# Performance work log

Hardware: AMD Instinct MI355X
Metric: run time of the kernel (lower is better)

The kernel has to match this reference:

```python
import jax, jax.numpy as jnp
from jax import lax
import numpy as np

NEG_INF = -1000000000.0  # matches torch masked_fill value
POS_THRESH = -100000000.0


def setup_inputs() -> dict:
    key = jax.random.key(0)
    k1, k2, k3 = jax.random.split(key, 3)
    B, C_in, L = 1, 16, 2048
    C_out, groups, K = 16, 4, 3
    scores = jax.random.normal(k1, (B, C_in, L, L), dtype=jnp.float32)
    weight = jax.random.normal(k2, (C_out, C_in // groups, K, K), dtype=jnp.float32) * 0.1
    bias = jax.random.normal(k3, (C_out,), dtype=jnp.float32) * 0.1
    return {"scores": scores, "weight": weight, "bias": bias}


def reference(scores, weight, bias):
    B, C_in, L, _ = scores.shape
    C_out, cpg, K, _ = weight.shape
    groups = C_in // cpg
    mask = jnp.tril(jnp.ones((L, L), dtype=bool))[None, None]  # (1,1,L,L) causal

    s = scores.astype(jnp.float32)
    z = jnp.where(mask, s, NEG_INF)

    # sparsemax over last axis: sort desc, cumsum, support-size threshold
    z_sorted = -jnp.sort(-z, axis=-1)                 # descending
    cum_sum = jnp.cumsum(z_sorted, axis=-1)
    k_idx = jnp.arange(1, L + 1, dtype=z.dtype)        # (L,) broadcasts over (B,C,L,L)
    cond = (1.0 + k_idx * z_sorted > cum_sum) & (z_sorted > POS_THRESH)
    k_sp = jnp.sum(cond, axis=-1, keepdims=True)       # support size, int
    k_safe = jnp.maximum(k_sp, 1)
    cum_sum_k = jnp.take_along_axis(cum_sum, k_safe - 1, axis=-1)
    tau = (cum_sum_k - 1.0) / k_safe.astype(z.dtype)
    tau = jnp.where(k_sp == 0, jnp.inf, tau)
    probs = jnp.maximum(z - tau, 0.0)                  # (B,C_in,L,L)

    # grouped same-padded conv2d over the (L,L) score map
    out = lax.conv_general_dilated(
        probs, weight,
        window_strides=(1, 1),
        padding=[(K // 2, K // 2), (K // 2, K // 2)],
        feature_group_count=groups,
        dimension_numbers=("NCHW", "OIHW", "NCHW"),
    )
    out = out + bias[None, :, None, None]
    out = jnp.where(mask, out, 0.0)
    return out.astype(scores.dtype)
```

## Files before the change

kernel.cpp:

```cpp
#include <hip/hip_runtime.h>

#define L 2048
#define CIN 16
#define GROUPS 4
#define NEG_INF  -1000000000.0f
#define POS_THRESH -100000000.0f

__global__ __launch_bounds__(256) void tau_kernel(const float* __restrict__ scores,
                                                  float* __restrict__ tau_out) {
    const int wid  = (blockIdx.x << 2) + (threadIdx.x >> 6);
    const int lane = threadIdx.x & 63;
    const int ws   = threadIdx.x >> 6;
    const int ch   = wid >> 11;
    const int row  = wid & 2047;
    const int n    = row + 1;
    const float* zrow = scores + ((size_t)ch * L + row) * L;

    float v[32];
    float m = NEG_INF;
#pragma unroll
    for (int j = 0; j < 8; ++j) {
        int c4 = lane + (j << 6);
        int c  = c4 << 2;
        float4 z = make_float4(NEG_INF, NEG_INF, NEG_INF, NEG_INF);
        if (c < n) z = *((const float4*)zrow + c4);
        v[4*j+0] = (c + 0 < n) ? z.x : NEG_INF;
        v[4*j+1] = (c + 1 < n) ? z.y : NEG_INF;
        v[4*j+2] = (c + 2 < n) ? z.z : NEG_INF;
        v[4*j+3] = (c + 3 < n) ? z.w : NEG_INF;
        m = fmaxf(m, fmaxf(fmaxf(v[4*j+0], v[4*j+1]), fmaxf(v[4*j+2], v[4*j+3])));
    }
#pragma unroll
    for (int d = 32; d; d >>= 1) m = fmaxf(m, __shfl_xor(m, d, 64));

    const float thr = m - 1.0f;

    __shared__ float buf[4][64];
    int base = 0;
#pragma unroll
    for (int j = 0; j < 32; ++j) {
        bool p = v[j] > thr;
        unsigned long long mask = __ballot(p);
        if (mask) {
            if (p) {
                int pos = __builtin_amdgcn_mbcnt_lo((unsigned)mask, 0);
                pos = __builtin_amdgcn_mbcnt_hi((unsigned)(mask >> 32), pos);
                pos += base;
                if (pos < 64) buf[ws][pos] = v[j];
            }
            base += __popcll(mask);
        }
    }
    __syncthreads();
    const int cnt = base;

    float tau;
    if (cnt <= 64) {
        float x = (lane < cnt) ? buf[ws][lane] : NEG_INF;
#pragma unroll
        for (int k = 2; k <= 64; k <<= 1) {
#pragma unroll
            for (int j = k >> 1; j > 0; j >>= 1) {
                float p = __shfl_xor(x, j, 64);
                bool desc    = ((lane & k) == 0);
                bool earlier = ((lane & j) == 0);
                float mx = fmaxf(x, p), mn = fminf(x, p);
                x = (desc == earlier) ? mx : mn;
            }
        }
        float csum = x;
#pragma unroll
        for (int d = 1; d < 64; d <<= 1) {
            float y = __shfl_up(csum, d, 64);
            if (lane >= d) csum += y;
        }
        bool cond = (1.0f + (float)(lane + 1) * x > csum) && (x > POS_THRESH);
        unsigned long long cmask = __ballot(cond);
        int k = (int)__popcll(cmask);
        float ck = __shfl(csum, k - 1, 64);
        tau = (ck - 1.0f) / (float)k;
    } else {
        tau = thr;
        int k_prev = -1;
        for (int it = 0; it < 64; ++it) {
            float S = 0.0f, Kf = 0.0f;
#pragma unroll
            for (int j = 0; j < 32; ++j)
                if (v[j] > tau) { S += v[j]; Kf += 1.0f; }
#pragma unroll
            for (int d = 32; d; d >>= 1) {
                S  += __shfl_xor(S,  d, 64);
                Kf += __shfl_xor(Kf, d, 64);
            }
            int K = (int)Kf;
            if (K == k_prev) break;
            tau = (S - 1.0f) / Kf;
            k_prev = K;
        }
    }
    if (lane == 0) tau_out[ch * L + row] = tau;
}

#define TR 16
#define TC 128
#define HR 18
#define PST 132

struct W6 { float l, m0, m1, m2, m3, r; };

__global__ __launch_bounds__(256, 4) void conv_kernel(const float* __restrict__ scores,
                                                      const float* __restrict__ tau,
                                                      const float* __restrict__ weight,
                                                      const float* __restrict__ bias,
                                                      float* __restrict__ out) {
    const int c0 = blockIdx.x * TC;
    const int r0 = blockIdx.y * TR;
    const int g  = blockIdx.z;
    const int t  = threadIdx.x;

    if (c0 > r0 + TR - 1) {
        const float4 z4 = make_float4(0.f, 0.f, 0.f, 0.f);
#pragma unroll
        for (int jj = 0; jj < 8; ++jj) {
            int idx = t + (jj << 8);
            int c4  = idx & 31;
            int r   = (idx >> 5) & 15;
            int o   = idx >> 9;
            float4* p = (float4*)(out + (((size_t)((g << 2) + o) * L + (r0 + r)) * L + c0)) + c4;
            *p = z4;
        }
        return;
    }

    __shared__ __align__(16) float P[4][HR][PST];

    const bool interior = (c0 >= 1) && (c0 + TC + 1 <= r0) && (r0 + TR <= L - 1);

    if (interior) {
        for (int ic = 0; ic < 4; ++ic) {
            const float* sb = scores + (size_t)((g << 2) + ic) * L * L;
            const float* tb = tau + ((g << 2) + ic) * L;
#pragma unroll
            for (int kk = 0; kk < 3; ++kk) {
                int idx = t + (kk << 8);
                if (idx < HR * 32) {
                    int hr = idx >> 5;
                    int c4 = idx & 31;
                    int r  = r0 - 1 + hr;
                    float tv = tb[r];
                    float4 z = *((const float4*)(sb + (size_t)r * L + c0) + c4);
                    float4 val;
                    val.x = fmaxf(z.x - tv, 0.f);
                    val.y = fmaxf(z.y - tv, 0.f);
                    val.z = fmaxf(z.z - tv, 0.f);
                    val.w = fmaxf(z.w - tv, 0.f);
                    *((float4*)&P[ic][hr][c4 << 2]) = val;
                }
            }
        }
        if (t < 144) {
            int side = t & 1, j = t >> 1;
            int ic = j / HR, hr = j - ic * HR;
            int r = r0 - 1 + hr;
            int c = side ? (c0 + TC) : (c0 - 1);
            float tv = tau[((g << 2) + ic) * L + r];
            float z  = scores[((size_t)((g << 2) + ic) * L + r) * L + c];
            P[ic][hr][side ? TC : 131] = fmaxf(z - tv, 0.f);
        }
    } else {
        for (int ic = 0; ic < 4; ++ic) {
            const float* sb = scores + (size_t)((g << 2) + ic) * L * L;
            const float* tb = tau + ((g << 2) + ic) * L;
#pragma unroll
            for (int kk = 0; kk < 3; ++kk) {
                int idx = t + (kk << 8);
                if (idx < HR * 32) {
                    int hr = idx >> 5;
                    int c4 = idx & 31;
                    int r  = r0 - 1 + hr;
                    int cb = c0 + (c4 << 2);
                    float4 val = make_float4(0.f, 0.f, 0.f, 0.f);
                    if (r >= 0 && r < L && cb <= r) {
                        float tv = tb[r];
                        float4 z = *((const float4*)(sb + (size_t)r * L) + (cb >> 2));
                        val.x = fmaxf(z.x - tv, 0.f);
                        val.y = (cb + 1 <= r) ? fmaxf(z.y - tv, 0.f) : 0.f;
                        val.z = (cb + 2 <= r) ? fmaxf(z.z - tv, 0.f) : 0.f;
                        val.w = (cb + 3 <= r) ? fmaxf(z.w - tv, 0.f) : 0.f;
                    }
                    *((float4*)&P[ic][hr][c4 << 2]) = val;
                }
            }
        }
        if (t < 144) {
            int side = t & 1, j = t >> 1;
            int ic = j / HR, hr = j - ic * HR;
            int r = r0 - 1 + hr;
            int c = side ? (c0 + TC) : (c0 - 1);
            float val = 0.f;
            if (r >= 0 && r < L && c >= 0 && c <= r) {
                val = fmaxf(scores[((size_t)((g << 2) + ic) * L + r) * L + c]
                            - tau[((g << 2) + ic) * L + r], 0.f);
            }
            P[ic][hr][side ? TC : 131] = val;
        }
    }
    __syncthreads();

    const int o    = __builtin_amdgcn_readfirstlane(t >> 6);
    const int lane = t & 63;
    const int col4 = lane & 31;
    const int rh   = lane >> 5;
    const int hb   = rh << 3;
    const int go   = (g << 2) + o;
    const int cb   = c0 + (col4 << 2);
    const int li   = col4 ? ((col4 << 2) - 2) : 130;
    const int ri   = (col4 << 2) + 4;

    float w[4][9];
#pragma unroll
    for (int ic = 0; ic < 4; ++ic)
#pragma unroll
        for (int k = 0; k < 9; ++k) w[ic][k] = weight[((go << 2) + ic) * 9 + k];
    const float bb = bias[go];

    auto ldwin = [&](int ic, int hr) -> W6 {
        const float* rp = &P[ic][hr][0];
        float4 M  = *(const float4*)(rp + (col4 << 2));
        float2 Lv = *(const float2*)(rp + li);
        float2 Rv = *(const float2*)(rp + ri);
        W6 q; q.l = Lv.y; q.m0 = M.x; q.m1 = M.y; q.m2 = M.z; q.m3 = M.w; q.r = Rv.x;
        return q;
    };

    float4 acc[8];
#pragma unroll
    for (int rr = 0; rr < 8; ++rr) acc[rr] = make_float4(bb, bb, bb, bb);

#pragma unroll
    for (int ic = 0; ic < 4; ++ic) {
        W6 a = ldwin(ic, hb);
        W6 b = ldwin(ic, hb + 1);
#pragma unroll
        for (int rr = 0; rr < 8; ++rr) {
            W6 c = ldwin(ic, hb + rr + 2);
            const W6 rows[3] = { a, b, c };
#pragma unroll
            for (int dy = 0; dy < 3; ++dy) {
                const W6& q = rows[dy];
                const float w0 = w[ic][dy * 3 + 0];
                const float w1 = w[ic][dy * 3 + 1];
                const float w2 = w[ic][dy * 3 + 2];
                acc[rr].x = fmaf(q.l,  w0, fmaf(q.m0, w1, fmaf(q.m1, w2, acc[rr].x)));
                acc[rr].y = fmaf(q.m0, w0, fmaf(q.m1, w1, fmaf(q.m2, w2, acc[rr].y)));
                acc[rr].z = fmaf(q.m1, w0, fmaf(q.m2, w1, fmaf(q.m3, w2, acc[rr].z)));
                acc[rr].w = fmaf(q.m2, w0, fmaf(q.m3, w1, fmaf(q.r,  w2, acc[rr].w)));
            }
            a = b; b = c;
        }
    }

    float* outp = out + ((size_t)go * L + (r0 + hb)) * L + cb;
    if (interior) {
#pragma unroll
        for (int rr = 0; rr < 8; ++rr)
            *(float4*)(outp + (size_t)rr * L) = acc[rr];
    } else {
#pragma unroll
        for (int rr = 0; rr < 8; ++rr) {
            int r = r0 + hb + rr;
            float4 res;
            res.x = (cb     <= r) ? acc[rr].x : 0.f;
            res.y = (cb + 1 <= r) ? acc[rr].y : 0.f;
            res.z = (cb + 2 <= r) ? acc[rr].z : 0.f;
            res.w = (cb + 3 <= r) ? acc[rr].w : 0.f;
            *(float4*)(outp + (size_t)rr * L) = res;
        }
    }
}

extern "C" void kernel_launch(void* const* d_in, const int* in_sizes, int n_in,
                              void* d_out, int out_size, void* d_ws, size_t ws_size,
                              hipStream_t stream) {
    const float* scores = (const float*)d_in[0];
    const float* weight = (const float*)d_in[1];
    const float* bias   = (const float*)d_in[2];
    float* out = (float*)d_out;
    float* tau = (float*)d_ws;

    tau_kernel<<<(CIN * L) / 4, 256, 0, stream>>>(scores, tau);

    dim3 gridB(L / TC, L / TR, GROUPS);
    conv_kernel<<<gridB, 256, 0, stream>>>(scores, tau, weight, bias, out);
}
```

Baseline: 526.0 us.

## Halve conv tile width and batch all halo loads before LDS writes

The conv tile shrinks from 128 to 64 columns, each thread now computes 4 rows instead of 8, and the launch-bound occupancy target rises from 4 to 8 blocks. Staging is restructured so every global load for all four input channels is issued into registers first, then converted and written to shared memory, which gives more memory-level parallelism per block. The aim is better latency hiding through higher occupancy and more loads in flight. The cost is a larger relative halo overhead per tile and more blocks to schedule.

Measured after the change: 496.3 us. -5.7%, faster.

```diff
diff --git a/kernel.cpp b/kernel.cpp
--- a/kernel.cpp
+++ b/kernel.cpp
@@ -102,13 +102,13 @@
 }
 
 #define TR 16
-#define TC 128
+#define TC 64
 #define HR 18
-#define PST 132
+#define PST 68
 
 struct W6 { float l, m0, m1, m2, m3, r; };
 
-__global__ __launch_bounds__(256, 4) void conv_kernel(const float* __restrict__ scores,
+__global__ __launch_bounds__(256, 8) void conv_kernel(const float* __restrict__ scores,
                                                       const float* __restrict__ tau,
                                                       const float* __restrict__ weight,
                                                       const float* __restrict__ bias,
@@ -121,11 +121,11 @@
     if (c0 > r0 + TR - 1) {
         const float4 z4 = make_float4(0.f, 0.f, 0.f, 0.f);
 #pragma unroll
-        for (int jj = 0; jj < 8; ++jj) {
-            int idx = t + (jj << 8);
-            int c4  = idx & 31;
-            int r   = (idx >> 5) & 15;
-            int o   = idx >> 9;
+        for (int jj = 0; jj < 4; ++jj) {
+            int idx = t + (jj << 8);
+            int c4  = idx & 15;
+            int r   = (idx >> 4) & 15;
+            int o   = idx >> 8;
             float4* p = (float4*)(out + (((size_t)((g << 2) + o) * L + (r0 + r)) * L + c0)) + c4;
             *p = z4;
         }
@@ -136,85 +136,107 @@
 
     const bool interior = (c0 >= 1) && (c0 + TC + 1 <= r0) && (r0 + TR <= L - 1);
 
+    const float* sbase = scores + (size_t)(g << 2) * L * L;
+    const float* tbase = tau + (g << 2) * L;
+
+    float4 zr[5];
+    float  tvr[5];
+
     if (interior) {
-        for (int ic = 0; ic < 4; ++ic) {
-            const float* sb = scores + (size_t)((g << 2) + ic) * L * L;
-            const float* tb = tau + ((g << 2) + ic) * L;
-#pragma unroll
-            for (int kk = 0; kk < 3; ++kk) {
-                int idx = t + (kk << 8);
-                if (idx < HR * 32) {
-                    int hr = idx >> 5;
-                    int c4 = idx & 31;
-                    int r  = r0 - 1 + hr;
-                    float tv = tb[r];
-                    float4 z = *((const float4*)(sb + (size_t)r * L + c0) + c4);
-                    float4 val;
+#pragma unroll
+        for (int jj = 0; jj < 5; ++jj) {
+            int idx = t + (jj << 8);
+            if (idx < 1152) {
+                int hr = idx >> 6, ic = (idx >> 4) & 3, c4 = idx & 15;
+                int r  = r0 - 1 + hr;
+                zr[jj]  = *((const float4*)(sbase + (size_t)ic * L * L + (size_t)r * L + c0) + c4);
+                tvr[jj] = tbase[ic * L + r];
+            }
+        }
+        float hv = 0.f;
+        int hic = 0, hhr = 0, hside = 0;
+        if (t < 144) {
+            hside = t & 1;
+            int j = t >> 1;
+            hic = j / HR; hhr = j - hic * HR;
+            int r = r0 - 1 + hhr;
+            int c = hside ? (c0 + TC) : (c0 - 1);
+            hv = fmaxf(sbase[(size_t)hic * L * L + (size_t)r * L + c] - tbase[hic * L + r], 0.f);
+        }
+#pragma unroll
+        for (int jj = 0; jj < 5; ++jj) {
+            int idx = t + (jj << 8);
+            if (idx < 1152) {
+                int hr = idx >> 6, ic = (idx >> 4) & 3, c4 = idx & 15;
+                float tv = tvr[jj];
+                float4 z = zr[jj];
+                float4 val;
+                val.x = fmaxf(z.x - tv, 0.f);
+                val.y = fmaxf(z.y - tv, 0.f);
+                val.z = fmaxf(z.z - tv, 0.f);
+                val.w = fmaxf(z.w - tv, 0.f);
+                *((float4*)&P[ic][hr][c4 << 2]) = val;
+            }
+        }
+        if (t < 144) P[hic][hhr][hside ? TC : 67] = hv;
+    } else {
+#pragma unroll
+        for (int jj = 0; jj < 5; ++jj) {
+            int idx = t + (jj << 8);
+            zr[jj] = make_float4(0.f, 0.f, 0.f, 0.f);
+            tvr[jj] = 0.f;
+            if (idx < 1152) {
+                int hr = idx >> 6, ic = (idx >> 4) & 3, c4 = idx & 15;
+                int r  = r0 - 1 + hr;
+                int cb = c0 + (c4 << 2);
+                if (r >= 0 && r < L && cb <= r) {
+                    zr[jj]  = *((const float4*)(sbase + (size_t)ic * L * L + (size_t)r * L) + (cb >> 2));
+                    tvr[jj] = tbase[ic * L + r];
+                }
+            }
+        }
+        float hv = 0.f;
+        int hic = 0, hhr = 0, hside = 0;
+        if (t < 144) {
+            hside = t & 1;
+            int j = t >> 1;
+            hic = j / HR; hhr = j - hic * HR;
+            int r = r0 - 1 + hhr;
+            int c = hside ? (c0 + TC) : (c0 - 1);
+            if (r >= 0 && r < L && c >= 0 && c <= r)
+                hv = fmaxf(sbase[(size_t)hic * L * L + (size_t)r * L + c] - tbase[hic * L + r], 0.f);
+        }
+#pragma unroll
+        for (int jj = 0; jj < 5; ++jj) {
+            int idx = t + (jj << 8);
+            if (idx < 1152) {
+                int hr = idx >> 6, ic = (idx >> 4) & 3, c4 = idx & 15;
+                int r  = r0 - 1 + hr;
+                int cb = c0 + (c4 << 2);
+                float tv = tvr[jj];
+                float4 z = zr[jj];
+                float4 val = make_float4(0.f, 0.f, 0.f, 0.f);
+                if (r >= 0 && r < L && cb <= r) {
                     val.x = fmaxf(z.x - tv, 0.f);
-                    val.y = fmaxf(z.y - tv, 0.f);
-                    val.z = fmaxf(z.z - tv, 0.f);
-                    val.w = fmaxf(z.w - tv, 0.f);
-                    *((float4*)&P[ic][hr][c4 << 2]) = val;
+                    val.y = (cb + 1 <= r) ? fmaxf(z.y - tv, 0.f) : 0.f;
+                    val.z = (cb + 2 <= r) ? fmaxf(z.z - tv, 0.f) : 0.f;
+                    val.w = (cb + 3 <= r) ? fmaxf(z.w - tv, 0.f) : 0.f;
                 }
-            }
-        }
-        if (t < 144) {
-            int side = t & 1, j = t >> 1;
-            int ic = j / HR, hr = j - ic * HR;
-            int r = r0 - 1 + hr;
-            int c = side ? (c0 + TC) : (c0 - 1);
-            float tv = tau[((g << 2) + ic) * L + r];
-            float z  = scores[((size_t)((g << 2) + ic) * L + r) * L + c];
-            P[ic][hr][side ? TC : 131] = fmaxf(z - tv, 0.f);
-        }
-    } else {
-        for (int ic = 0; ic < 4; ++ic) {
-            const float* sb = scores + (size_t)((g << 2) + ic) * L * L;
-            const float* tb = tau + ((g << 2) + ic) * L;
-#pragma unroll
-            for (int kk = 0; kk < 3; ++kk) {
-                int idx = t + (kk << 8);
-                if (idx < HR * 32) {
-                    int hr = idx >> 5;
-                    int c4 = idx & 31;
-                    int r  = r0 - 1 + hr;
-                    int cb = c0 + (c4 << 2);
-                    float4 val = make_float4(0.f, 0.f, 0.f, 0.f);
-                    if (r >= 0 && r < L && cb <= r) {
-                        float tv = tb[r];
-                        float4 z = *((const float4*)(sb + (size_t)r * L) + (cb >> 2));
-                        val.x = fmaxf(z.x - tv, 0.f);
-                        val.y = (cb + 1 <= r) ? fmaxf(z.y - tv, 0.f) : 0.f;
-                        val.z = (cb + 2 <= r) ? fmaxf(z.z - tv, 0.f) : 0.f;
-                        val.w = (cb + 3 <= r) ? fmaxf(z.w - tv, 0.f) : 0.f;
-                    }
-                    *((float4*)&P[ic][hr][c4 << 2]) = val;
-                }
-            }
-        }
-        if (t < 144) {
-            int side = t & 1, j = t >> 1;
-            int ic = j / HR, hr = j - ic * HR;
-            int r = r0 - 1 + hr;
-            int c = side ? (c0 + TC) : (c0 - 1);
-            float val = 0.f;
-            if (r >= 0 && r < L && c >= 0 && c <= r) {
-                val = fmaxf(scores[((size_t)((g << 2) + ic) * L + r) * L + c]
-                            - tau[((g << 2) + ic) * L + r], 0.f);
-            }
-            P[ic][hr][side ? TC : 131] = val;
-        }
+                *((float4*)&P[ic][hr][c4 << 2]) = val;
+            }
+        }
+        if (t < 144) P[hic][hhr][hside ? TC : 67] = hv;
     }
     __syncthreads();
 
     const int o    = __builtin_amdgcn_readfirstlane(t >> 6);
     const int lane = t & 63;
-    const int col4 = lane & 31;
-    const int rh   = lane >> 5;
-    const int hb   = rh << 3;
+    const int col4 = lane & 15;
+    const int rq   = lane >> 4;
+    const int hb   = rq << 2;
     const int go   = (g << 2) + o;
     const int cb   = c0 + (col4 << 2);
-    const int li   = col4 ? ((col4 << 2) - 2) : 130;
+    const int li   = col4 ? ((col4 << 2) - 2) : 66;
     const int ri   = (col4 << 2) + 4;
 
     float w[4][9];
@@ -233,16 +255,16 @@
         return q;
     };
 
-    float4 acc[8];
-#pragma unroll
-    for (int rr = 0; rr < 8; ++rr) acc[rr] = make_float4(bb, bb, bb, bb);
+    float4 acc[4];
+#pragma unroll
+    for (int rr = 0; rr < 4; ++rr) acc[rr] = make_float4(bb, bb, bb, bb);
 
 #pragma unroll
     for (int ic = 0; ic < 4; ++ic) {
         W6 a = ldwin(ic, hb);
         W6 b = ldwin(ic, hb + 1);
 #pragma unroll
-        for (int rr = 0; rr < 8; ++rr) {
+        for (int rr = 0; rr < 4; ++rr) {
             W6 c = ldwin(ic, hb + rr + 2);
             const W6 rows[3] = { a, b, c };
 #pragma unroll
@@ -263,11 +285,11 @@
     float* outp = out + ((size_t)go * L + (r0 + hb)) * L + cb;
     if (interior) {
 #pragma unroll
-        for (int rr = 0; rr < 8; ++rr)
+        for (int rr = 0; rr < 4; ++rr)
             *(float4*)(outp + (size_t)rr * L) = acc[rr];
     } else {
 #pragma unroll
-        for (int rr = 0; rr < 8; ++rr) {
+        for (int rr = 0; rr < 4; ++rr) {
             int r = r0 + hb + rr;
             float4 res;
             res.x = (cb     <= r) ? acc[rr].x : 0.f;
```
